# Performance work log

Measured on AMD Instinct MI355X. Metric: run time of the kernel, lower is better.

Reference implementation:

```python
import jax, jax.numpy as jnp
import numpy as np

B, T, C, H = 4, 2048, 1024, 16
D = C // H  # head_dim = 64
ROPE_BASE = 10000.0


def _rope_cos_sin(T, D, dtype):
    # inv_freq: (D/2,), freqs: (T, D/2) -> cos/sin tiled to (T, D)
    inv_freq = 1.0 / (ROPE_BASE ** (jnp.arange(0, D, 2, dtype=jnp.float32) / D))
    freqs = jnp.arange(T, dtype=jnp.float32)[:, None] * inv_freq[None, :]
    emb = jnp.concatenate([freqs, freqs], axis=-1)  # (T, D)
    return jnp.cos(emb).astype(dtype), jnp.sin(emb).astype(dtype)


def _rotate_half(x):
    x1, x2 = jnp.split(x, 2, axis=-1)
    return jnp.concatenate([-x2, x1], axis=-1)


def setup_inputs() -> dict:
    key = jax.random.key(0)
    k1, k2, k3 = jax.random.split(key, 3)
    x = jax.random.normal(k1, (B, T, C), dtype=jnp.float32)
    W_qkv = jax.random.normal(k2, (C, 3 * C), dtype=jnp.float32) * (C ** -0.5)
    b_qkv = jnp.zeros((3 * C,), dtype=jnp.float32)
    W_out = jax.random.normal(k3, (C, C), dtype=jnp.float32) * (C ** -0.5)
    b_out = jnp.zeros((C,), dtype=jnp.float32)
    return {"x": x, "W_qkv": W_qkv, "b_qkv": b_qkv, "W_out": W_out, "b_out": b_out}


def reference(x, W_qkv, b_qkv, W_out, b_out):
    Bx, Tx, Cx = x.shape
    qkv = x @ W_qkv + b_qkv                                   # (B, T, 3C)
    qkv = qkv.reshape(Bx, Tx, 3, H, D).transpose(2, 0, 3, 1, 4)  # (3, B, H, T, D)
    q, k, v = qkv[0], qkv[1], qkv[2]

    cos, sin = _rope_cos_sin(Tx, D, x.dtype)                  # (T, D) each
    q = q * cos + _rotate_half(q) * sin
    k = k * cos + _rotate_half(k) * sin

    # NOTE: original code has no 1/sqrt(D) scaling — faithful reproduction.
    att = jnp.einsum('bhtd,bhsd->bhts', q, k)                 # (B, H, T, T)
    causal = jnp.tril(jnp.ones((Tx, Tx), dtype=bool))
    att = jnp.where(causal[None, None, :, :], att, -jnp.inf)
    att = jax.nn.softmax(att, axis=-1)
    y = jnp.einsum('bhts,bhsd->bhtd', att, v)                 # (B, H, T, D)
    y = y.transpose(0, 2, 1, 3).reshape(Bx, Tx, Cx)
    return y @ W_out + b_out
```

## Files before the change

kernel.cpp:

```cpp
#include <hip/hip_runtime.h>
#include <math.h>

#define NB    4
#define T_SEQ 2048
#define CDIM  1024
#define NH    16
#define DH    64
#define NQKV  3072

typedef short bf16x8 __attribute__((ext_vector_type(8)));
typedef float f32x4  __attribute__((ext_vector_type(4)));

#define GLOBAL_AS __attribute__((address_space(1)))
#define LDS_AS    __attribute__((address_space(3)))

__device__ __forceinline__ void async16(const void* g, void* l) {
  __builtin_amdgcn_global_load_lds((const GLOBAL_AS void*)g, (LDS_AS void*)l, 16, 0, 0);
}

__device__ __forceinline__ unsigned short f2bf(float f) {
  unsigned u = __float_as_uint(f);
  unsigned r = u + 0x7FFF + ((u >> 16) & 1);
  return (unsigned short)(r >> 16);
}

#define SWZ8(row, c) ((((row) << 3) | ((c) ^ ((row) & 7))) << 3)

#define BARRIER()  asm volatile("s_barrier" ::: "memory")
#define VMCNT(n)   asm volatile("s_waitcnt vmcnt(" #n ")" ::: "memory")

__device__ __forceinline__ void transpose_tile32(
    const float* __restrict__ in, unsigned short* __restrict__ out,
    int K, int N, int bx, int by, float (*tile)[33], int tid) {
  int n0 = bx << 5, k0 = by << 5;
  int r  = tid >> 3;
  int c4 = (tid & 7) << 2;
  float4 v = *(const float4*)&in[(size_t)(k0 + r) * N + n0 + c4];
  tile[r][c4 + 0] = v.x; tile[r][c4 + 1] = v.y;
  tile[r][c4 + 2] = v.z; tile[r][c4 + 3] = v.w;
  __syncthreads();
  ushort4 o;
  o.x = f2bf(tile[c4 + 0][r]); o.y = f2bf(tile[c4 + 1][r]);
  o.z = f2bf(tile[c4 + 2][r]); o.w = f2bf(tile[c4 + 3][r]);
  *(ushort4*)&out[(size_t)(n0 + r) * K + k0 + c4] = o;
}

__global__ __launch_bounds__(256) void prep_fused(
    const float* __restrict__ x, unsigned short* __restrict__ xb,
    const float* __restrict__ W_qkv, unsigned short* __restrict__ wqt,
    const float* __restrict__ W_out, unsigned short* __restrict__ wot,
    float2* __restrict__ rope) {
  __shared__ float tile[32][33];
  int blk = blockIdx.x;
  int tid = threadIdx.x;
  if (blk < 8192) {
    int i = blk * 256 + tid;
    float4 v = ((const float4*)x)[i];
    ushort4 o;
    o.x = f2bf(v.x); o.y = f2bf(v.y); o.z = f2bf(v.z); o.w = f2bf(v.w);
    ((ushort4*)xb)[i] = o;
  } else if (blk < 11264) {
    int local = blk - 8192;
    transpose_tile32(W_qkv, wqt, CDIM, NQKV, local % 96, local / 96, tile, tid);
  } else if (blk < 12288) {
    int local = blk - 11264;
    transpose_tile32(W_out, wot, CDIM, CDIM, local & 31, local >> 5, tile, tid);
  } else {
    int i = (blk - 12288) * 256 + tid;
    int t = i >> 5, d = i & 31;
    float inv = expf((float)d * -0.28782313662425572f);
    float s, c;
    sincosf((float)t * inv, &s, &c);
    rope[i] = make_float2(c, s);
  }
}

__global__ __launch_bounds__(256) void transpose_v(
    const unsigned short* __restrict__ v, unsigned short* __restrict__ vt) {
  __shared__ unsigned short tile[64][65];
  int bh = blockIdx.y;
  int t0 = blockIdx.x << 6;
  size_t ib = (size_t)bh * (T_SEQ * DH);
  int tid = threadIdx.x;
#pragma unroll
  for (int u = 0; u < 2; ++u) {
    int f = u * 256 + tid;
    int tr = f >> 3, c = f & 7;
    bf16x8 val = *(const bf16x8*)&v[ib + (size_t)(t0 + tr) * DH + c * 8];
#pragma unroll
    for (int j = 0; j < 8; ++j) tile[tr][c * 8 + j] = (unsigned short)val[j];
  }
  __syncthreads();
#pragma unroll
  for (int u = 0; u < 2; ++u) {
    int f = u * 256 + tid;
    int d = f >> 3, c = f & 7;
    bf16x8 o;
#pragma unroll
    for (int j = 0; j < 8; ++j) o[j] = (short)tile[c * 8 + j][d];
    *(bf16x8*)&vt[ib + (size_t)d * T_SEQ + t0 + c * 8] = o;
  }
}

#define STAGE(kt, b)                                                          \
  { const unsigned short* sa_ = aSrc + (kt) * 64;                             \
    const unsigned short* sb_ = bSrc + (kt) * 64;                             \
    async16(sa_,          &As[b][d0]);                                        \
    async16(sa_ + 65536,  &As[b][d0 + 4096]);                                 \
    async16(sb_,          &Bs[b][d0]);                                        \
    async16(sb_ + 65536,  &Bs[b][d0 + 4096]);                                 \
    async16(sb_ + 131072, &Bs[b][d0 + 8192]);                                 \
    async16(sb_ + 196608, &Bs[b][d0 + 12288]); }

#define GEMM_PIPE(Aptr, Btptr)                                                \
  int tid = threadIdx.x;                                                      \
  int wave = tid >> 6, lane = tid & 63;                                       \
  int wm = wave >> 2, wn = wave & 3;                                          \
  int col = lane & 15, quad = lane >> 4;                                      \
  int srow = tid >> 3;                                                        \
  int schunk = (tid & 7) ^ (srow & 7);                                        \
  const unsigned short* aSrc = &Aptr[(size_t)(m0 + srow) * CDIM + schunk * 8];\
  const unsigned short* bSrc = &Btptr[(size_t)(n0 + srow) * CDIM + schunk * 8];\
  int d0 = wave * 512;      \
  f32x4 acc[4][4];                                                            \
  _Pragma("unroll") for (int mt = 0; mt < 4; ++mt)                            \
  _Pragma("unroll") for (int nt = 0; nt < 4; ++nt)                            \
    acc[mt][nt] = (f32x4){0.f, 0.f, 0.f, 0.f};                                \
  STAGE(0, 0)                                                                 \
  STAGE(1, 1)                                                                 \
  _Pragma("unroll")                                                           \
  for (int t = 0; t < 16; ++t) {                                              \
    if (t < 15) { VMCNT(6); } else { VMCNT(0); }                              \
    BARRIER();                                                                \
    if (t + 2 < 16) STAGE(t + 2, (t + 2) % 3)                                 \
    const short* A_ = As[t % 3];                                              \
    const short* B_ = Bs[t % 3];                                              \
    _Pragma("unroll") for (int ks = 0; ks < 2; ++ks) {                        \
      bf16x8 af[4], bfr[4];                                                   \
      _Pragma("unroll") for (int mt = 0; mt < 4; ++mt)                        \
        af[mt] = *(const bf16x8*)&A_[SWZ8(wm * 64 + mt * 16 + col,            \
                                          ks * 4 + quad)];                    \
      _Pragma("unroll") for (int nt = 0; nt < 4; ++nt)                        \
        bfr[nt] = *(const bf16x8*)&B_[SWZ8(wn * 64 + nt * 16 + col,           \
                                           ks * 4 + quad)];                   \
      __builtin_amdgcn_s_setprio(1);                                          \
      _Pragma("unroll") for (int mt = 0; mt < 4; ++mt)                        \
        _Pragma("unroll") for (int nt = 0; nt < 4; ++nt)                      \
          acc[mt][nt] = __builtin_amdgcn_mfma_f32_16x16x32_bf16(              \
              af[mt], bfr[nt], acc[mt][nt], 0, 0, 0);                         \
      __builtin_amdgcn_s_setprio(0);                                          \
    }                                                                         \
  }

__global__ __launch_bounds__(512, 2) void gemm_qkv_mfma(
    const unsigned short* __restrict__ A, const unsigned short* __restrict__ Bt,
    const float* __restrict__ bias, const float2* __restrict__ rope,
    unsigned short* __restrict__ qb, unsigned short* __restrict__ kb,
    unsigned short* __restrict__ vb) {
  __shared__ short As[3][128 * 64];
  __shared__ short Bs[3][256 * 64];
  int orig = blockIdx.x;
  int wg = (orig & 7) * 96 + (orig >> 3);
  int m0 = (wg / 12) << 7, n0 = (wg % 12) << 8;
  GEMM_PIPE(A, Bt)
  int nn = n0 + wn * 64;
  int which = nn >> 10;
  int h = (nn >> 6) & 15;
  unsigned short* dst = (which == 0) ? qb : ((which == 1) ? kb : vb);
  float bv[4];
#pragma unroll
  for (int nt = 0; nt < 4; ++nt) bv[nt] = bias[nn + nt * 16 + col];
  if (which < 2) {
#pragma unroll
    for (int mt = 0; mt < 4; ++mt) {
#pragma unroll
      for (int r = 0; r < 4; ++r) {
        int m = m0 + wm * 64 + mt * 16 + quad * 4 + r;
        int bidx = m >> 11, t = m & 2047;
        float x0 = acc[mt][0][r] + bv[0];
        float x1 = acc[mt][1][r] + bv[1];
        float x2 = acc[mt][2][r] + bv[2];
        float x3 = acc[mt][3][r] + bv[3];
        float2 cs0 = rope[(t << 5) + col];
        float2 cs1 = rope[(t << 5) + col + 16];
        size_t ro = (((size_t)bidx * NH + h) * T_SEQ + t) * DH;
        dst[ro + col]      = f2bf(x0 * cs0.x - x2 * cs0.y);
        dst[ro + col + 16] = f2bf(x1 * cs1.x - x3 * cs1.y);
        dst[ro + col + 32] = f2bf(x2 * cs0.x + x0 * cs0.y);
        dst[ro + col + 48] = f2bf(x3 * cs1.x + x1 * cs1.y);
      }
    }
  } else {
#pragma unroll
    for (int mt = 0; mt < 4; ++mt) {
#pragma unroll
      for (int r = 0; r < 4; ++r) {
        int m = m0 + wm * 64 + mt * 16 + quad * 4 + r;
        int bidx = m >> 11, t = m & 2047;
        size_t ro = (((size_t)bidx * NH + h) * T_SEQ + t) * DH;
        dst[ro + col]      = f2bf(acc[mt][0][r] + bv[0]);
        dst[ro + col + 16] = f2bf(acc[mt][1][r] + bv[1]);
        dst[ro + col + 32] = f2bf(acc[mt][2][r] + bv[2]);
        dst[ro + col + 48] = f2bf(acc[mt][3][r] + bv[3]);
      }
    }
  }
}

__global__ __launch_bounds__(512, 2) void gemm_out_mfma(
    const unsigned short* __restrict__ A, const unsigned short* __restrict__ Bt,
    const float* __restrict__ bias, float* __restrict__ out) {
  __shared__ short As[3][128 * 64];
  __shared__ short Bs[3][256 * 64];
  int orig = blockIdx.x;
  int wg = (orig & 7) * 32 + (orig >> 3);
  int m0 = (wg >> 2) << 7, n0 = (wg & 3) << 8;
  GEMM_PIPE(A, Bt)
#pragma unroll
  for (int nt = 0; nt < 4; ++nt) {
    int n = n0 + wn * 64 + nt * 16 + col;
    float bv = bias[n];
#pragma unroll
    for (int mt = 0; mt < 4; ++mt) {
#pragma unroll
      for (int r = 0; r < 4; ++r) {
        int m = m0 + wm * 64 + mt * 16 + quad * 4 + r;
        out[(size_t)m * CDIM + n] = acc[mt][nt][r] + bv;
      }
    }
  }
}

__global__ __launch_bounds__(256) void attn_mfma(
    const unsigned short* __restrict__ qg, const unsigned short* __restrict__ kg,
    const unsigned short* __restrict__ vtg, unsigned short* __restrict__ yb) {
  __shared__ short Ks[2][64 * 64];
  __shared__ short Vts[2][64 * 64];
  __shared__ short Ps[4][32 * 64];
  int tid = threadIdx.x;
  int wave = tid >> 6, lane = tid & 63;
  int col = lane & 15, quad = lane >> 4;
  int bh = blockIdx.x;
  int qblk = 15 - (int)blockIdx.y;
  int qb0 = qblk << 7;
  size_t base = (size_t)bh * (T_SEQ * DH);

  bf16x8 qreg[2][2];
#pragma unroll
  for (int nt = 0; nt < 2; ++nt)
#pragma unroll
    for (int kc = 0; kc < 2; ++kc)
      qreg[nt][kc] = *(const bf16x8*)&qg[base +
          (size_t)(qb0 + wave * 32 + nt * 16 + col) * DH + kc * 32 + quad * 8];

  bf16x8 ones;
#pragma unroll
  for (int j = 0; j < 8; ++j) ones[j] = (short)0x3F80;

  f32x4 oc[2][4], lsum[2];
#pragma unroll
  for (int mq = 0; mq < 2; ++mq) {
    lsum[mq] = (f32x4){0.f, 0.f, 0.f, 0.f};
#pragma unroll
    for (int dt = 0; dt < 4; ++dt) oc[mq][dt] = (f32x4){0.f, 0.f, 0.f, 0.f};
  }

  int qlo = qb0 + wave * 32;
  int qhi = qlo + 31;
  int nrounds = qblk + 1;
  for (int rr = 0; rr < nrounds; ++rr) {
    __syncthreads();
#pragma unroll
    for (int v = 0; v < 2; ++v) {
      int s_ = (rr * 2 + v) << 6;
#pragma unroll
      for (int u = 0; u < 2; ++u) {
        int ff = u * 256 + wave * 64 + lane;
        int row = ff >> 3, cl = ff & 7;
        int cg = cl ^ (row & 7);
        async16(&kg[base + (size_t)(s_ + row) * DH + cg * 8],
                &Ks[v][(u * 256 + wave * 64) * 8]);
        async16(&vtg[base + (size_t)row * T_SEQ + s_ + cg * 8],
                &Vts[v][(u * 256 + wave * 64) * 8]);
      }
    }
    __syncthreads();

#pragma unroll
    for (int v = 0; v < 2; ++v) {
      int kb = rr * 2 + v;
      int s0 = kb << 6;
      if (s0 > qhi) continue;
      const short* K_ = Ks[v];
      const short* V_ = Vts[v];

      f32x4 sc[4][2];
#pragma unroll
      for (int mf = 0; mf < 4; ++mf)
#pragma unroll
        for (int nt = 0; nt < 2; ++nt) sc[mf][nt] = (f32x4){0.f, 0.f, 0.f, 0.f};
#pragma unroll
      for (int kc = 0; kc < 2; ++kc) {
#pragma unroll
        for (int mf = 0; mf < 4; ++mf) {
          bf16x8 ak = *(const bf16x8*)&K_[SWZ8(mf * 16 + col, kc * 4 + quad)];
          sc[mf][0] = __builtin_amdgcn_mfma_f32_16x16x32_bf16(ak, qreg[0][kc], sc[mf][0], 0, 0, 0);
          sc[mf][1] = __builtin_amdgcn_mfma_f32_16x16x32_bf16(ak, qreg[1][kc], sc[mf][1], 0, 0, 0);
        }
      }

      if (s0 + 63 > qlo) {
#pragma unroll
        for (int mf = 0; mf < 4; ++mf) {
          int kbase = s0 + mf * 16 + quad * 4;
#pragma unroll
          for (int nt = 0; nt < 2; ++nt) {
            int qq = qlo + nt * 16 + col;
#pragma unroll
            for (int r = 0; r < 4; ++r)
              if (kbase + r > qq) sc[mf][nt][r] = -3.0e38f;
          }
        }
      }

#pragma unroll
      for (int nt = 0; nt < 2; ++nt) {
        int row = nt * 16 + col;
        int rb = row << 6;
        int sw = row & 7;
#pragma unroll
        for (int mf = 0; mf < 4; ++mf) {
          float p0 = __expf(sc[mf][nt][0]);
          float p1 = __expf(sc[mf][nt][1]);
          float p2 = __expf(sc[mf][nt][2]);
          float p3 = __expf(sc[mf][nt][3]);
          unsigned w0, w1;
          asm("v_cvt_pk_bf16_f32 %0, %1, %2" : "=v"(w0) : "v"(p0), "v"(p1));
          asm("v_cvt_pk_bf16_f32 %0, %1, %2" : "=v"(w1) : "v"(p2), "v"(p3));
          int chunk = (mf << 1) | (quad >> 1);
          int off = rb + (((chunk ^ sw) << 3) | ((quad & 1) << 2));
          *(uint2*)&Ps[wave][off] = make_uint2(w0, w1);
        }
      }

#pragma unroll
      for (int kc = 0; kc < 2; ++kc) {
        bf16x8 ap0 = *(const bf16x8*)&Ps[wave][SWZ8(col,      kc * 4 + quad)];
        bf16x8 ap1 = *(const bf16x8*)&Ps[wave][SWZ8(16 + col, kc * 4 + quad)];
        lsum[0] = __builtin_amdgcn_mfma_f32_16x16x32_bf16(ap0, ones, lsum[0], 0, 0, 0);
        lsum[1] = __builtin_amdgcn_mfma_f32_16x16x32_bf16(ap1, ones, lsum[1], 0, 0, 0);
#pragma unroll
        for (int dt = 0; dt < 4; ++dt) {
          bf16x8 vb = *(const bf16x8*)&V_[SWZ8(dt * 16 + col, kc * 4 + quad)];
          oc[0][dt] = __builtin_amdgcn_mfma_f32_16x16x32_bf16(ap0, vb, oc[0][dt], 0, 0, 0);
          oc[1][dt] = __builtin_amdgcn_mfma_f32_16x16x32_bf16(ap1, vb, oc[1][dt], 0, 0, 0);
        }
      }
    }
  }

  int b = bh >> 4, h = bh & 15;
#pragma unroll
  for (int mq = 0; mq < 2; ++mq)
#pragma unroll
    for (int dt = 0; dt < 4; ++dt) {
      int d = dt * 16 + col;
#pragma unroll
      for (int r = 0; r < 4; ++r) {
        int t = qb0 + wave * 32 + mq * 16 + quad * 4 + r;
        yb[(((size_t)b * T_SEQ + t) * NH + h) * DH + d] =
            f2bf(oc[mq][dt][r] / lsum[mq][r]);
      }
    }
}

extern "C" void kernel_launch(void* const* d_in, const int* in_sizes, int n_in,
                              void* d_out, int out_size, void* d_ws, size_t ws_size,
                              hipStream_t stream) {
  const float* x     = (const float*)d_in[0];
  const float* W_qkv = (const float*)d_in[1];
  const float* b_qkv = (const float*)d_in[2];
  const float* W_out = (const float*)d_in[3];
  const float* b_out = (const float*)d_in[4];
  float* out = (float*)d_out;

  const size_t per = (size_t)NB * NH * T_SEQ * DH;
  unsigned short* xb  = (unsigned short*)d_ws;
  unsigned short* qb  = xb + per;
  unsigned short* kbf = qb + per;
  unsigned short* vbf = kbf + per;
  unsigned short* vtb = vbf + per;
  unsigned short* yb  = vtb + per;
  unsigned short* wqt = yb + per;
  unsigned short* wot = wqt + (size_t)NQKV * CDIM;
  float2* rope = (float2*)(wot + (size_t)CDIM * CDIM);

  prep_fused<<<12544, 256, 0, stream>>>(x, xb, W_qkv, wqt, W_out, wot, rope);
  gemm_qkv_mfma<<<768, 512, 0, stream>>>(xb, wqt, b_qkv, rope, qb, kbf, vbf);
  transpose_v<<<dim3(T_SEQ / 64, NB * NH), 256, 0, stream>>>(vbf, vtb);
  attn_mfma<<<dim3(NB * NH, T_SEQ / 128), 256, 0, stream>>>(qb, kbf, vtb, yb);
  gemm_out_mfma<<<256, 512, 0, stream>>>(yb, wot, b_out, out);
}
```

Measured before the change: 247.3 us.

## Fuse V transpose into QKV GEMM epilogue via LDS staging

The standalone transpose_v kernel is removed. The QKV GEMM epilogue now stages V outputs through per-wave LDS tiles and writes them directly in the transposed (B,H,D,T) layout with 16-byte stores. This drops a kernel launch and a full read/write pass over V, at the cost of an extra barrier and LDS traffic in the epilogue for V-producing blocks.

```diff
diff --git a/kernel.cpp b/kernel.cpp
--- a/kernel.cpp
+++ b/kernel.cpp
@@ -72,33 +72,6 @@
     float s, c;
     sincosf((float)t * inv, &s, &c);
     rope[i] = make_float2(c, s);
-  }
-}
-
-__global__ __launch_bounds__(256) void transpose_v(
-    const unsigned short* __restrict__ v, unsigned short* __restrict__ vt) {
-  __shared__ unsigned short tile[64][65];
-  int bh = blockIdx.y;
-  int t0 = blockIdx.x << 6;
-  size_t ib = (size_t)bh * (T_SEQ * DH);
-  int tid = threadIdx.x;
-#pragma unroll
-  for (int u = 0; u < 2; ++u) {
-    int f = u * 256 + tid;
-    int tr = f >> 3, c = f & 7;
-    bf16x8 val = *(const bf16x8*)&v[ib + (size_t)(t0 + tr) * DH + c * 8];
-#pragma unroll
-    for (int j = 0; j < 8; ++j) tile[tr][c * 8 + j] = (unsigned short)val[j];
-  }
-  __syncthreads();
-#pragma unroll
-  for (int u = 0; u < 2; ++u) {
-    int f = u * 256 + tid;
-    int d = f >> 3, c = f & 7;
-    bf16x8 o;
-#pragma unroll
-    for (int j = 0; j < 8; ++j) o[j] = (short)tile[c * 8 + j][d];
-    *(bf16x8*)&vt[ib + (size_t)d * T_SEQ + t0 + c * 8] = o;
   }
 }
 
@@ -156,7 +129,7 @@
     const unsigned short* __restrict__ A, const unsigned short* __restrict__ Bt,
     const float* __restrict__ bias, const float2* __restrict__ rope,
     unsigned short* __restrict__ qb, unsigned short* __restrict__ kb,
-    unsigned short* __restrict__ vb) {
+    unsigned short* __restrict__ vtb) {
   __shared__ short As[3][128 * 64];
   __shared__ short Bs[3][256 * 64];
   int orig = blockIdx.x;
@@ -166,11 +139,11 @@
   int nn = n0 + wn * 64;
   int which = nn >> 10;
   int h = (nn >> 6) & 15;
-  unsigned short* dst = (which == 0) ? qb : ((which == 1) ? kb : vb);
   float bv[4];
 #pragma unroll
   for (int nt = 0; nt < 4; ++nt) bv[nt] = bias[nn + nt * 16 + col];
   if (which < 2) {
+    unsigned short* dst = (which == 0) ? qb : kb;
 #pragma unroll
     for (int mt = 0; mt < 4; ++mt) {
 #pragma unroll
@@ -191,18 +164,32 @@
       }
     }
   } else {
-#pragma unroll
-    for (int mt = 0; mt < 4; ++mt) {
-#pragma unroll
-      for (int r = 0; r < 4; ++r) {
-        int m = m0 + wm * 64 + mt * 16 + quad * 4 + r;
-        int bidx = m >> 11, t = m & 2047;
-        size_t ro = (((size_t)bidx * NH + h) * T_SEQ + t) * DH;
-        dst[ro + col]      = f2bf(acc[mt][0][r] + bv[0]);
-        dst[ro + col + 16] = f2bf(acc[mt][1][r] + bv[1]);
-        dst[ro + col + 32] = f2bf(acc[mt][2][r] + bv[2]);
-        dst[ro + col + 48] = f2bf(acc[mt][3][r] + bv[3]);
-      }
+    BARRIER();
+    short* vt_tile = &Bs[0][0] + wave * (64 * 72);
+#pragma unroll
+    for (int nt = 0; nt < 4; ++nt) {
+#pragma unroll
+      for (int mt = 0; mt < 4; ++mt) {
+        float y0 = acc[mt][nt][0] + bv[nt];
+        float y1 = acc[mt][nt][1] + bv[nt];
+        float y2 = acc[mt][nt][2] + bv[nt];
+        float y3 = acc[mt][nt][3] + bv[nt];
+        unsigned w0, w1;
+        asm("v_cvt_pk_bf16_f32 %0, %1, %2" : "=v"(w0) : "v"(y0), "v"(y1));
+        asm("v_cvt_pk_bf16_f32 %0, %1, %2" : "=v"(w1) : "v"(y2), "v"(y3));
+        *(uint2*)&vt_tile[(nt * 16 + col) * 72 + mt * 16 + quad * 4] =
+            make_uint2(w0, w1);
+      }
+    }
+    int mbase = m0 + wm * 64;
+    int bidx = mbase >> 11, t0v = mbase & 2047;
+    size_t vbase = ((size_t)(bidx * NH + h) * DH) * T_SEQ;
+#pragma unroll
+    for (int u = 0; u < 8; ++u) {
+      int f = u * 64 + lane;
+      int d = f >> 3, c = f & 7;
+      bf16x8 o = *(const bf16x8*)&vt_tile[d * 72 + c * 8];
+      *(bf16x8*)&vtb[vbase + (size_t)d * T_SEQ + t0v + c * 8] = o;
     }
   }
 }
@@ -396,8 +383,7 @@
   float2* rope = (float2*)(wot + (size_t)CDIM * CDIM);
 
   prep_fused<<<12544, 256, 0, stream>>>(x, xb, W_qkv, wqt, W_out, wot, rope);
-  gemm_qkv_mfma<<<768, 512, 0, stream>>>(xb, wqt, b_qkv, rope, qb, kbf, vbf);
-  transpose_v<<<dim3(T_SEQ / 64, NB * NH), 256, 0, stream>>>(vbf, vtb);
+  gemm_qkv_mfma<<<768, 512, 0, stream>>>(xb, wqt, b_qkv, rope, qb, kbf, vtb);
   attn_mfma<<<dim3(NB * NH, T_SEQ / 128), 256, 0, stream>>>(qb, kbf, vtb, yb);
   gemm_out_mfma<<<256, 512, 0, stream>>>(yb, wot, b_out, out);
 }
```

Result: faster. 236.5 us (median of 3 runs) (-4.4%).
